# Kernel tuning notes

Measured on AMD Instinct MI355X. Metric: run time of the kernel, lower is better.

Reference implementation:

```python
import jax, jax.numpy as jnp
import numpy as np

A_DIM = 12      # action dim (half of augmented state)
N_STEPS = 10    # Heun ODE steps (Flow.N)
P = 0.95        # mixing coefficient in _Heun_method


def _mlp(x, obs, t, W1, b1, W2, b2, W3, b3, W4, b4):
    h = jnp.concatenate([x, obs, t], axis=-1)
    h = jnp.tanh(h @ W1 + b1)
    h = jnp.tanh(h @ W2 + b2)
    h = jnp.tanh(h @ W3 + b3)
    return h @ W4 + b4


def _heun(obs, x, params):
    # Flow._Heun_method: sequential Heun integration of the augmented state.
    z = x[..., :A_DIM]
    y = x[..., A_DIM:]
    dt = 1.0 / N_STEPS
    tshape = x.shape[:-1] + (1,)

    def step(carry, i):
        z, y = carry
        t = jnp.ones(tshape, x.dtype) * (i / N_STEPS)
        z_t = _mlp(y, obs, t, *params)
        z_in = z + z_t * dt
        y_t = _mlp(z_in, obs, t, *params)
        y_in = y + y_t * dt
        z_new = P * z_in + (1.0 - P) * y_in
        y_new = P * y_in + (1.0 - P) * z_new
        return (z_new, y_new), None

    (z, y), _ = jax.lax.scan(step, (z, y), jnp.arange(N_STEPS, dtype=x.dtype))
    return jnp.concatenate([z, y], axis=-1)


def setup_inputs() -> dict:
    key = jax.random.key(0)
    ks = jax.random.split(key, 8)
    B, OBS, H, A = 2048, 48, 256, A_DIM
    din = A + OBS + 1  # 61
    s = 0.05  # small init scale to keep tanh unsaturated
    return {
        "observations": jax.random.normal(ks[0], (B, OBS), jnp.float32),
        "action_aug_0": jax.random.normal(ks[1], (B, 2 * A), jnp.float32),
        "W1": s * jax.random.normal(ks[2], (din, H), jnp.float32),
        "b1": jnp.zeros((H,), jnp.float32),
        "W2": s * jax.random.normal(ks[3], (H, H), jnp.float32),
        "b2": jnp.zeros((H,), jnp.float32),
        "W3": s * jax.random.normal(ks[4], (H, H), jnp.float32),
        "b3": jnp.zeros((H,), jnp.float32),
        "W4": s * jax.random.normal(ks[5], (H, A), jnp.float32),
        "b4": jnp.zeros((A,), jnp.float32),
        "jac": 1,
    }


def reference(observations, action_aug_0, W1, b1, W2, b2, W3, b3, W4, b4, jac):
    params = (W1, b1, W2, b2, W3, b3, W4, b4)
    action_aug = _heun(observations, action_aug_0, params)
    d = action_aug_0.shape[-1]
    # Normal(0, I) log prob summed over dims
    log_probs = -0.5 * jnp.sum(action_aug_0 ** 2, axis=-1) - 0.5 * d * jnp.log(2.0 * jnp.pi)
    if jac:
        single = lambda o, x: _heun(o, x, params)  # per-sample (obs_dim,), (2a,)
        J = jax.vmap(jax.jacrev(single, argnums=1))(observations, action_aug_0)  # (B, 2a, 2a)
        _, logabsdet = jnp.linalg.slogdet(J)  # = log|det J|
        log_probs = log_probs - logabsdet
    return action_aug, log_probs
```

## Files before the change

### kernel.cpp

```cpp
#include <hip/hip_runtime.h>
#include <hip/hip_bf16.h>


typedef unsigned short ushort_t;
typedef float f32x4 __attribute__((ext_vector_type(4)));
typedef short s16x8 __attribute__((ext_vector_type(8)));

#define NB      2048
#define OBS_D   48
#define XDIM    24
#define NSTEPS  10
#define DT      0.1f
#define PP      0.95f
#define SCL     2.885390081777927f

#define W1U  0
#define W2U  16384
#define W3U  81920
#define W4U  147456
#define W1AU 151552
#define FRAG_BLOCKS 624
#define LP_BLOCKS 8

#define LDS_BUFA 0
#define LDS_BUFB 8192
#define LDS_AIN  16384
#define LDS_PART 17408
#define LDS_TOTAL 25600

__device__ __forceinline__ ushort_t f2bf(float f) {
  unsigned u = __builtin_bit_cast(unsigned, f);
  u += 0x7fffu + ((u >> 16) & 1u);
  return (ushort_t)(u >> 16);
}

__device__ __forceinline__ float tanh_s(float u) {
  float e = __builtin_amdgcn_exp2f(u);
  return __builtin_fmaf(-2.f, __builtin_amdgcn_rcpf(1.f + e), 1.f);
}

__device__ __forceinline__ int pair_byte(int c) {
  return (((c >> 5) << 6) | ((c & 15) << 2) | (((c >> 4) & 1) << 1));
}

__global__ void prep_kernel(const float* __restrict__ W1, const float* __restrict__ b1,
                            const float* __restrict__ W2, const float* __restrict__ W3,
                            const float* __restrict__ W4, const float* __restrict__ x0,
                            const int* __restrict__ jac, float* __restrict__ out,
                            ushort_t* __restrict__ ws) {
  int bid = blockIdx.x;
  int tid = threadIdx.x;
  if (bid < FRAG_BLOCKS) {
    int e = bid * 256 + tid;
    float val = 0.f;
    if (e < 16384) {
      int kt = e >> 13; int r = e & 8191;
      int nt = r >> 9, l = (r >> 3) & 63, j = r & 7;
      int k = kt * 32 + ((l >> 4) << 2) + (j >> 1) + ((j & 1) << 4);
      int col = nt * 16 + (l & 15);
      val = SCL * ((k < 61) ? W1[k * 256 + col] : ((k == 61) ? b1[col] : 0.f));
    } else if (e < 81920) {
      int e2 = e - 16384;
      int kt = e2 >> 13; int r = e2 & 8191;
      int nt = r >> 9, l = (r >> 3) & 63, j = r & 7;
      int k = kt * 32 + ((l >> 4) << 2) + (j >> 1) + ((j & 1) << 4);
      val = SCL * W2[k * 256 + nt * 16 + (l & 15)];
    } else if (e < 147456) {
      int e2 = e - 81920;
      int kt = e2 >> 13; int r = e2 & 8191;
      int nt = r >> 9, l = (r >> 3) & 63, j = r & 7;
      int k = kt * 32 + ((l >> 4) << 2) + (j >> 1) + ((j & 1) << 4);
      val = SCL * W3[k * 256 + nt * 16 + (l & 15)];
    } else if (e < 151552) {
      int e2 = e - 147456;
      int kt = e2 >> 9; int r = e2 & 511;
      int l = (r >> 3) & 63, j = r & 7;
      int k = kt * 32 + ((l >> 4) << 2) + (j >> 1) + ((j & 1) << 4);
      int col = l & 15;
      val = (col < 12) ? W4[k * 12 + col] : 0.f;
    } else {
      int e2 = e - 151552;
      int nt = e2 >> 9; int r = e2 & 511;
      int l = (r >> 3) & 63, j = r & 7;
      int k = ((l >> 4) << 2) + (j >> 1) + ((j & 1) << 4);
      val = (k < 12) ? SCL * W1[k * 256 + nt * 16 + (l & 15)] : 0.f;
    }
    ws[e] = f2bf(val);
  } else {
    int s = (bid - FRAG_BLOCKS) * 256 + tid;
    float acc = 0.f;
    #pragma unroll 4
    for (int j = 0; j < XDIM; ++j) { float v = x0[s * XDIM + j]; acc += v * v; }
    float C = (jac[0] != 0) ? -9.744134143900015f : -22.054524796912143f;
    out[NB * XDIM + s] = -0.5f * acc + C;
  }
}

__global__ __launch_bounds__(512, 2) void flow_main(
    const float* __restrict__ obs, const float* __restrict__ x0,
    const float* __restrict__ W1g, const float* __restrict__ b2g,
    const float* __restrict__ b3g, const float* __restrict__ b4g,
    const ushort_t* __restrict__ ws, float* __restrict__ out) {
  __shared__ char lds[LDS_TOTAL];
  const int tid  = threadIdx.x;
  const int lane = tid & 63;
  const int wv   = tid >> 6;
  const int g    = lane >> 4;
  const int ar   = lane & 15;
  const int row0 = blockIdx.x * 16;
  const int sw   = (ar & 7) << 4;
  const int rs   = tid >> 4, cs = tid & 15;

  int roff[8];
  #pragma unroll
  for (int c = 0; c < 8; ++c)
    roff[c] = ar * 512 + (((((wv + c) & 7) * 64) + g * 16) ^ sw);
  int woff[4], pwoff[4];
  #pragma unroll
  for (int r = 0; r < 4; ++r) {
    int rw = 4 * g + r;
    woff[r]  = rw * 512 + ((wv * 64 + ar * 4) ^ ((rw & 7) << 4));
    pwoff[r] = LDS_PART + ((rw * 128 + ar * 8 + (wv ^ (g << 1))) << 2);
  }

  ((unsigned*)(lds + LDS_BUFB))[tid] = 0u;
  if (tid < 256) ((unsigned*)(lds + LDS_AIN))[tid] = 0u;
  __syncthreads();

  for (int idx = tid; idx < 16 * OBS_D; idx += 512) {
    int r = idx / OBS_D, o = idx - r * OBS_D;
    int byt = pair_byte(12 + o) ^ ((r & 7) << 4);
    *(ushort_t*)(lds + LDS_BUFB + r * 128 + byt) = f2bf(obs[(row0 + r) * OBS_D + o]);
  }
  if (tid < 16)
    *(ushort_t*)(lds + LDS_BUFB + tid * 128 + (pair_byte(61) ^ ((tid & 7) << 4))) = (ushort_t)0x3F80;

  float zr = 0.f, yr = 0.f, zir = 0.f;
  if (tid < 256 && cs < 12) {
    zr = x0[(row0 + rs) * XDIM + cs];
    yr = x0[(row0 + rs) * XDIM + 12 + cs];
    *(ushort_t*)(lds + LDS_AIN + rs * 64 + ((cs * 4) ^ ((rs & 3) << 4))) = f2bf(yr);
  }

  s16x8 w1o[2][2], w1a[2], w2r[8][2], w3r[8][2], w4r;
  #pragma unroll
  for (int kt = 0; kt < 2; ++kt)
    #pragma unroll
    for (int n = 0; n < 2; ++n)
      w1o[kt][n] = *(const s16x8*)(ws + W1U + (((kt * 16) + (2 * wv + n)) * 64 + lane) * 8);
  #pragma unroll
  for (int n = 0; n < 2; ++n)
    w1a[n] = *(const s16x8*)(ws + W1AU + ((2 * wv + n) * 64 + lane) * 8);
  #pragma unroll
  for (int c = 0; c < 8; ++c) {
    int kt = (wv + c) & 7;
    #pragma unroll
    for (int n = 0; n < 2; ++n) {
      w2r[c][n] = *(const s16x8*)(ws + W2U + (((kt * 16) + (2 * wv + n)) * 64 + lane) * 8);
      w3r[c][n] = *(const s16x8*)(ws + W3U + (((kt * 16) + (2 * wv + n)) * 64 + lane) * 8);
    }
  }
  w4r = *(const s16x8*)(ws + W4U + (wv * 64 + lane) * 8);
  asm volatile("" : "+v"(w1a[0]), "+v"(w1a[1]), "+v"(w4r));
  #pragma unroll
  for (int c = 0; c < 8; ++c)
    asm volatile("" : "+v"(w2r[c][0]), "+v"(w2r[c][1]), "+v"(w3r[c][0]), "+v"(w3r[c][1]));

  const float w1t0 = SCL * W1g[60 * 256 + 32 * wv + ar];
  const float w1t1 = SCL * W1g[60 * 256 + 32 * wv + 16 + ar];
  const float b2s0 = SCL * b2g[32 * wv + ar],      b2s1 = SCL * b2g[32 * wv + 16 + ar];
  const float b3s0 = SCL * b3g[32 * wv + ar],      b3s1 = SCL * b3g[32 * wv + 16 + ar];
  const float b4v  = (cs < 12) ? b4g[cs] : 0.f;

  __syncthreads();

  const f32x4 z4 = {0.f, 0.f, 0.f, 0.f};
  f32x4 ci0 = z4, ci1 = z4;
  #pragma unroll
  for (int kt = 0; kt < 2; ++kt) {
    s16x8 a = *(const s16x8*)(lds + LDS_BUFB + ar * 128 + ((kt * 64 + g * 16) ^ sw));
    ci0 = __builtin_amdgcn_mfma_f32_16x16x32_bf16(a, w1o[kt][0], ci0, 0, 0, 0);
    ci1 = __builtin_amdgcn_mfma_f32_16x16x32_bf16(a, w1o[kt][1], ci1, 0, 0, 0);
  }

  for (int i = 0; i < NSTEPS; ++i) {
    const float t = (float)i * DT;
    const float t0 = t * w1t0, t1 = t * w1t1;
    #pragma unroll
    for (int ev = 0; ev < 2; ++ev) {
      f32x4 acc0 = ci0, acc1 = ci1;
      #pragma unroll
      for (int r = 0; r < 4; ++r) { acc0[r] += t0; acc1[r] += t1; }
      {
        s16x8 a = *(const s16x8*)(lds + LDS_AIN + ar * 64 + ((g * 16) ^ ((ar & 3) << 4)));
        acc0 = __builtin_amdgcn_mfma_f32_16x16x32_bf16(a, w1a[0], acc0, 0, 0, 0);
        acc1 = __builtin_amdgcn_mfma_f32_16x16x32_bf16(a, w1a[1], acc1, 0, 0, 0);
      }
      #pragma unroll
      for (int r = 0; r < 4; ++r) {
        unsigned p;
        float lo = tanh_s(acc0[r]), hi = tanh_s(acc1[r]);
        asm("v_cvt_pk_bf16_f32 %0, %1, %2" : "=v"(p) : "v"(lo), "v"(hi));
        *(unsigned*)(lds + LDS_BUFA + woff[r]) = p;
      }
      __syncthreads();

      f32x4 c0[4], c1[4];
      c0[0] = (f32x4){b2s0, b2s0, b2s0, b2s0}; c1[0] = (f32x4){b2s1, b2s1, b2s1, b2s1};
      c0[1] = z4; c0[2] = z4; c0[3] = z4; c1[1] = z4; c1[2] = z4; c1[3] = z4;
      __builtin_amdgcn_s_setprio(1);
      #pragma unroll
      for (int c = 0; c < 4; ++c) {
        s16x8 a = *(const s16x8*)(lds + LDS_BUFA + roff[c]);
        s16x8 b = *(const s16x8*)(lds + LDS_BUFA + roff[c + 4]);
        c0[c] = __builtin_amdgcn_mfma_f32_16x16x32_bf16(a, w2r[c][0], c0[c], 0, 0, 0);
        c1[c] = __builtin_amdgcn_mfma_f32_16x16x32_bf16(a, w2r[c][1], c1[c], 0, 0, 0);
        c0[c] = __builtin_amdgcn_mfma_f32_16x16x32_bf16(b, w2r[c + 4][0], c0[c], 0, 0, 0);
        c1[c] = __builtin_amdgcn_mfma_f32_16x16x32_bf16(b, w2r[c + 4][1], c1[c], 0, 0, 0);
      }
      __builtin_amdgcn_s_setprio(0);
      acc0 = (c0[0] + c0[1]) + (c0[2] + c0[3]);
      acc1 = (c1[0] + c1[1]) + (c1[2] + c1[3]);
      #pragma unroll
      for (int r = 0; r < 4; ++r) {
        unsigned p;
        float lo = tanh_s(acc0[r]), hi = tanh_s(acc1[r]);
        asm("v_cvt_pk_bf16_f32 %0, %1, %2" : "=v"(p) : "v"(lo), "v"(hi));
        *(unsigned*)(lds + LDS_BUFB + woff[r]) = p;
      }
      __syncthreads();

      c0[0] = (f32x4){b3s0, b3s0, b3s0, b3s0}; c1[0] = (f32x4){b3s1, b3s1, b3s1, b3s1};
      c0[1] = z4; c0[2] = z4; c0[3] = z4; c1[1] = z4; c1[2] = z4; c1[3] = z4;
      __builtin_amdgcn_s_setprio(1);
      #pragma unroll
      for (int c = 0; c < 4; ++c) {
        s16x8 a = *(const s16x8*)(lds + LDS_BUFB + roff[c]);
        s16x8 b = *(const s16x8*)(lds + LDS_BUFB + roff[c + 4]);
        c0[c] = __builtin_amdgcn_mfma_f32_16x16x32_bf16(a, w3r[c][0], c0[c], 0, 0, 0);
        c1[c] = __builtin_amdgcn_mfma_f32_16x16x32_bf16(a, w3r[c][1], c1[c], 0, 0, 0);
        c0[c] = __builtin_amdgcn_mfma_f32_16x16x32_bf16(b, w3r[c + 4][0], c0[c], 0, 0, 0);
        c1[c] = __builtin_amdgcn_mfma_f32_16x16x32_bf16(b, w3r[c + 4][1], c1[c], 0, 0, 0);
      }
      __builtin_amdgcn_s_setprio(0);
      acc0 = (c0[0] + c0[1]) + (c0[2] + c0[3]);
      acc1 = (c1[0] + c1[1]) + (c1[2] + c1[3]);
      #pragma unroll
      for (int r = 0; r < 4; ++r) {
        unsigned p;
        float lo = tanh_s(acc0[r]), hi = tanh_s(acc1[r]);
        asm("v_cvt_pk_bf16_f32 %0, %1, %2" : "=v"(p) : "v"(lo), "v"(hi));
        *(unsigned*)(lds + LDS_BUFA + woff[r]) = p;
      }

      asm volatile("s_waitcnt lgkmcnt(0)" ::: "memory");
      __builtin_amdgcn_sched_barrier(0);
      {
        s16x8 a = *(const s16x8*)(lds + LDS_BUFA + roff[0]);
        f32x4 p4 = __builtin_amdgcn_mfma_f32_16x16x32_bf16(a, w4r, z4, 0, 0, 0);
        #pragma unroll
        for (int r = 0; r < 4; ++r)
          *(float*)(lds + pwoff[r]) = p4[r];
      }
      __syncthreads();

      if (tid < 256) {
        const char* pb = lds + LDS_PART + ((rs * 128 + cs * 8) << 2);
        f32x4 va = *(const f32x4*)pb;
        f32x4 vb = *(const f32x4*)(pb + 16);
        f32x4 sv = va + vb;
        float s = ((sv[0] + sv[1]) + (sv[2] + sv[3])) + b4v;
        if (cs < 12) {
          int byt = rs * 64 + ((cs * 4) ^ ((rs & 3) << 4));
          if (ev == 0) {
            zir = zr + DT * s;
            *(ushort_t*)(lds + LDS_AIN + byt) = f2bf(zir);
          } else {
            float yi = yr + DT * s;
            zr = PP * zir + (1.f - PP) * yi;
            yr = PP * yi + (1.f - PP) * zr;
            *(ushort_t*)(lds + LDS_AIN + byt) = f2bf(yr);
          }
        }
      }
      __syncthreads();
    }
  }

  if (tid < 256 && cs < 12) {
    out[(row0 + rs) * XDIM + cs]      = zr;
    out[(row0 + rs) * XDIM + 12 + cs] = yr;
  }
}

extern "C" void kernel_launch(void* const* d_in, const int* in_sizes, int n_in,
                              void* d_out, int out_size, void* d_ws, size_t ws_size,
                              hipStream_t stream) {
  const float* obs = (const float*)d_in[0];
  const float* x0  = (const float*)d_in[1];
  const float* W1  = (const float*)d_in[2];
  const float* b1  = (const float*)d_in[3];
  const float* W2  = (const float*)d_in[4];
  const float* b2  = (const float*)d_in[5];
  const float* W3  = (const float*)d_in[6];
  const float* b3  = (const float*)d_in[7];
  const float* W4  = (const float*)d_in[8];
  const float* b4  = (const float*)d_in[9];
  const int*   jac = (const int*)d_in[10];
  float* out = (float*)d_out;
  ushort_t* ws = (ushort_t*)d_ws;

  prep_kernel<<<FRAG_BLOCKS + LP_BLOCKS, 256, 0, stream>>>(W1, b1, W2, W3, W4, x0, jac, out, ws);
  flow_main<<<128, 512, 0, stream>>>(obs, x0, W1, b2, b3, b4, ws, out);
}
```

Baseline: 47.20 us.

## Process two 16-row tiles per block to reuse register-resident weights

Each 512-thread block now handles 32 batch rows as two 16-row tiles instead of one, so the grid is halved. Per layer, the MFMAs and tanh work for both tiles are interleaved, which reuses the weight fragments already held in registers and gives independent MFMA chains to hide latency across each barrier. LDS buffers are doubled to hold both tiles, and every thread now takes part in the state update. The cost is half as many blocks on a large GPU, leaving fewer CUs busy, along with more registers and more LDS per block.

```diff
diff --git a/kernel.cpp b/kernel.cpp
--- a/kernel.cpp
+++ b/kernel.cpp
@@ -13,6 +13,7 @@
 #define DT      0.1f
 #define PP      0.95f
 #define SCL     2.885390081777927f
+#define TILES   2
 
 #define W1U  0
 #define W2U  16384
@@ -23,10 +24,10 @@
 #define LP_BLOCKS 8
 
 #define LDS_BUFA 0
-#define LDS_BUFB 8192
-#define LDS_AIN  16384
-#define LDS_PART 17408
-#define LDS_TOTAL 25600
+#define LDS_BUFB 16384
+#define LDS_AIN  32768
+#define LDS_PART 34816
+#define LDS_TOTAL 51200
 
 __device__ __forceinline__ ushort_t f2bf(float f) {
   unsigned u = __builtin_bit_cast(unsigned, f);
@@ -107,9 +108,9 @@
   const int wv   = tid >> 6;
   const int g    = lane >> 4;
   const int ar   = lane & 15;
-  const int row0 = blockIdx.x * 16;
+  const int row0 = blockIdx.x * (16 * TILES);
   const int sw   = (ar & 7) << 4;
-  const int rs   = tid >> 4, cs = tid & 15;
+  const int tt   = tid >> 8, rs = (tid >> 4) & 15, cs = tid & 15;
 
   int roff[8];
   #pragma unroll
@@ -123,23 +124,33 @@
     pwoff[r] = LDS_PART + ((rw * 128 + ar * 8 + (wv ^ (g << 1))) << 2);
   }
 
-  ((unsigned*)(lds + LDS_BUFB))[tid] = 0u;
-  if (tid < 256) ((unsigned*)(lds + LDS_AIN))[tid] = 0u;
+  {
+    unsigned* z1 = (unsigned*)(lds + LDS_BUFB);
+    unsigned* z2 = (unsigned*)(lds + LDS_BUFB + 8192);
+    if (tid < 512) { z1[tid] = 0u; z2[tid] = 0u; }
+    ((unsigned*)(lds + LDS_AIN))[tid] = 0u;
+  }
   __syncthreads();
 
-  for (int idx = tid; idx < 16 * OBS_D; idx += 512) {
-    int r = idx / OBS_D, o = idx - r * OBS_D;
+  for (int idx = tid; idx < TILES * 16 * OBS_D; idx += 512) {
+    int t = idx / (16 * OBS_D);
+    int rem = idx - t * (16 * OBS_D);
+    int r = rem / OBS_D, o = rem - r * OBS_D;
     int byt = pair_byte(12 + o) ^ ((r & 7) << 4);
-    *(ushort_t*)(lds + LDS_BUFB + r * 128 + byt) = f2bf(obs[(row0 + r) * OBS_D + o]);
-  }
-  if (tid < 16)
-    *(ushort_t*)(lds + LDS_BUFB + tid * 128 + (pair_byte(61) ^ ((tid & 7) << 4))) = (ushort_t)0x3F80;
+    *(ushort_t*)(lds + LDS_BUFB + t * 8192 + r * 128 + byt) =
+        f2bf(obs[(row0 + t * 16 + r) * OBS_D + o]);
+  }
+  if (tid < 16 * TILES) {
+    int t = tid >> 4, r = tid & 15;
+    *(ushort_t*)(lds + LDS_BUFB + t * 8192 + r * 128 + (pair_byte(61) ^ ((r & 7) << 4))) =
+        (ushort_t)0x3F80;
+  }
 
   float zr = 0.f, yr = 0.f, zir = 0.f;
-  if (tid < 256 && cs < 12) {
-    zr = x0[(row0 + rs) * XDIM + cs];
-    yr = x0[(row0 + rs) * XDIM + 12 + cs];
-    *(ushort_t*)(lds + LDS_AIN + rs * 64 + ((cs * 4) ^ ((rs & 3) << 4))) = f2bf(yr);
+  if (cs < 12) {
+    zr = x0[(row0 + tt * 16 + rs) * XDIM + cs];
+    yr = x0[(row0 + tt * 16 + rs) * XDIM + 12 + cs];
+    *(ushort_t*)(lds + LDS_AIN + tt * 1024 + rs * 64 + ((cs * 4) ^ ((rs & 3) << 4))) = f2bf(yr);
   }
 
   s16x8 w1o[2][2], w1a[2], w2r[8][2], w3r[8][2], w4r;
@@ -175,12 +186,16 @@
   __syncthreads();
 
   const f32x4 z4 = {0.f, 0.f, 0.f, 0.f};
-  f32x4 ci0 = z4, ci1 = z4;
-  #pragma unroll
-  for (int kt = 0; kt < 2; ++kt) {
-    s16x8 a = *(const s16x8*)(lds + LDS_BUFB + ar * 128 + ((kt * 64 + g * 16) ^ sw));
-    ci0 = __builtin_amdgcn_mfma_f32_16x16x32_bf16(a, w1o[kt][0], ci0, 0, 0, 0);
-    ci1 = __builtin_amdgcn_mfma_f32_16x16x32_bf16(a, w1o[kt][1], ci1, 0, 0, 0);
+  f32x4 ci0[TILES], ci1[TILES];
+  #pragma unroll
+  for (int t = 0; t < TILES; ++t) {
+    ci0[t] = z4; ci1[t] = z4;
+    #pragma unroll
+    for (int kt = 0; kt < 2; ++kt) {
+      s16x8 a = *(const s16x8*)(lds + LDS_BUFB + t * 8192 + ar * 128 + ((kt * 64 + g * 16) ^ sw));
+      ci0[t] = __builtin_amdgcn_mfma_f32_16x16x32_bf16(a, w1o[kt][0], ci0[t], 0, 0, 0);
+      ci1[t] = __builtin_amdgcn_mfma_f32_16x16x32_bf16(a, w1o[kt][1], ci1[t], 0, 0, 0);
+    }
   }
 
   for (int i = 0; i < NSTEPS; ++i) {
@@ -188,90 +203,112 @@
     const float t0 = t * w1t0, t1 = t * w1t1;
     #pragma unroll
     for (int ev = 0; ev < 2; ++ev) {
-      f32x4 acc0 = ci0, acc1 = ci1;
-      #pragma unroll
-      for (int r = 0; r < 4; ++r) { acc0[r] += t0; acc1[r] += t1; }
-      {
-        s16x8 a = *(const s16x8*)(lds + LDS_AIN + ar * 64 + ((g * 16) ^ ((ar & 3) << 4)));
-        acc0 = __builtin_amdgcn_mfma_f32_16x16x32_bf16(a, w1a[0], acc0, 0, 0, 0);
-        acc1 = __builtin_amdgcn_mfma_f32_16x16x32_bf16(a, w1a[1], acc1, 0, 0, 0);
-      }
-      #pragma unroll
-      for (int r = 0; r < 4; ++r) {
-        unsigned p;
-        float lo = tanh_s(acc0[r]), hi = tanh_s(acc1[r]);
-        asm("v_cvt_pk_bf16_f32 %0, %1, %2" : "=v"(p) : "v"(lo), "v"(hi));
-        *(unsigned*)(lds + LDS_BUFA + woff[r]) = p;
-      }
+      f32x4 acc0[TILES], acc1[TILES];
+      #pragma unroll
+      for (int tl = 0; tl < TILES; ++tl) {
+        acc0[tl] = ci0[tl]; acc1[tl] = ci1[tl];
+        #pragma unroll
+        for (int r = 0; r < 4; ++r) { acc0[tl][r] += t0; acc1[tl][r] += t1; }
+        s16x8 a = *(const s16x8*)(lds + LDS_AIN + tl * 1024 + ar * 64 +
+                                  ((g * 16) ^ ((ar & 3) << 4)));
+        acc0[tl] = __builtin_amdgcn_mfma_f32_16x16x32_bf16(a, w1a[0], acc0[tl], 0, 0, 0);
+        acc1[tl] = __builtin_amdgcn_mfma_f32_16x16x32_bf16(a, w1a[1], acc1[tl], 0, 0, 0);
+      }
+      #pragma unroll
+      for (int tl = 0; tl < TILES; ++tl)
+        #pragma unroll
+        for (int r = 0; r < 4; ++r) {
+          unsigned p;
+          float lo = tanh_s(acc0[tl][r]), hi = tanh_s(acc1[tl][r]);
+          asm("v_cvt_pk_bf16_f32 %0, %1, %2" : "=v"(p) : "v"(lo), "v"(hi));
+          *(unsigned*)(lds + LDS_BUFA + tl * 8192 + woff[r]) = p;
+        }
       __syncthreads();
 
-      f32x4 c0[4], c1[4];
-      c0[0] = (f32x4){b2s0, b2s0, b2s0, b2s0}; c1[0] = (f32x4){b2s1, b2s1, b2s1, b2s1};
-      c0[1] = z4; c0[2] = z4; c0[3] = z4; c1[1] = z4; c1[2] = z4; c1[3] = z4;
+      f32x4 A0a[TILES], A0b[TILES], A1a[TILES], A1b[TILES];
+      #pragma unroll
+      for (int tl = 0; tl < TILES; ++tl) {
+        A0a[tl] = (f32x4){b2s0, b2s0, b2s0, b2s0};
+        A1a[tl] = (f32x4){b2s1, b2s1, b2s1, b2s1};
+        A0b[tl] = z4; A1b[tl] = z4;
+      }
       __builtin_amdgcn_s_setprio(1);
       #pragma unroll
-      for (int c = 0; c < 4; ++c) {
-        s16x8 a = *(const s16x8*)(lds + LDS_BUFA + roff[c]);
-        s16x8 b = *(const s16x8*)(lds + LDS_BUFA + roff[c + 4]);
-        c0[c] = __builtin_amdgcn_mfma_f32_16x16x32_bf16(a, w2r[c][0], c0[c], 0, 0, 0);
-        c1[c] = __builtin_amdgcn_mfma_f32_16x16x32_bf16(a, w2r[c][1], c1[c], 0, 0, 0);
-        c0[c] = __builtin_amdgcn_mfma_f32_16x16x32_bf16(b, w2r[c + 4][0], c0[c], 0, 0, 0);
-        c1[c] = __builtin_amdgcn_mfma_f32_16x16x32_bf16(b, w2r[c + 4][1], c1[c], 0, 0, 0);
-      }
+      for (int c = 0; c < 4; ++c)
+        #pragma unroll
+        for (int tl = 0; tl < TILES; ++tl) {
+          s16x8 a = *(const s16x8*)(lds + LDS_BUFA + tl * 8192 + roff[c]);
+          s16x8 b = *(const s16x8*)(lds + LDS_BUFA + tl * 8192 + roff[c + 4]);
+          A0a[tl] = __builtin_amdgcn_mfma_f32_16x16x32_bf16(a, w2r[c][0], A0a[tl], 0, 0, 0);
+          A1a[tl] = __builtin_amdgcn_mfma_f32_16x16x32_bf16(a, w2r[c][1], A1a[tl], 0, 0, 0);
+          A0b[tl] = __builtin_amdgcn_mfma_f32_16x16x32_bf16(b, w2r[c + 4][0], A0b[tl], 0, 0, 0);
+          A1b[tl] = __builtin_amdgcn_mfma_f32_16x16x32_bf16(b, w2r[c + 4][1], A1b[tl], 0, 0, 0);
+        }
       __builtin_amdgcn_s_setprio(0);
-      acc0 = (c0[0] + c0[1]) + (c0[2] + c0[3]);
-      acc1 = (c1[0] + c1[1]) + (c1[2] + c1[3]);
-      #pragma unroll
-      for (int r = 0; r < 4; ++r) {
-        unsigned p;
-        float lo = tanh_s(acc0[r]), hi = tanh_s(acc1[r]);
-        asm("v_cvt_pk_bf16_f32 %0, %1, %2" : "=v"(p) : "v"(lo), "v"(hi));
-        *(unsigned*)(lds + LDS_BUFB + woff[r]) = p;
+      #pragma unroll
+      for (int tl = 0; tl < TILES; ++tl) {
+        acc0[tl] = A0a[tl] + A0b[tl]; acc1[tl] = A1a[tl] + A1b[tl];
+        #pragma unroll
+        for (int r = 0; r < 4; ++r) {
+          unsigned p;
+          float lo = tanh_s(acc0[tl][r]), hi = tanh_s(acc1[tl][r]);
+          asm("v_cvt_pk_bf16_f32 %0, %1, %2" : "=v"(p) : "v"(lo), "v"(hi));
+          *(unsigned*)(lds + LDS_BUFB + tl * 8192 + woff[r]) = p;
+        }
       }
       __syncthreads();
 
-      c0[0] = (f32x4){b3s0, b3s0, b3s0, b3s0}; c1[0] = (f32x4){b3s1, b3s1, b3s1, b3s1};
-      c0[1] = z4; c0[2] = z4; c0[3] = z4; c1[1] = z4; c1[2] = z4; c1[3] = z4;
+      #pragma unroll
+      for (int tl = 0; tl < TILES; ++tl) {
+        A0a[tl] = (f32x4){b3s0, b3s0, b3s0, b3s0};
+        A1a[tl] = (f32x4){b3s1, b3s1, b3s1, b3s1};
+        A0b[tl] = z4; A1b[tl] = z4;
+      }
       __builtin_amdgcn_s_setprio(1);
       #pragma unroll
-      for (int c = 0; c < 4; ++c) {
-        s16x8 a = *(const s16x8*)(lds + LDS_BUFB + roff[c]);
-        s16x8 b = *(const s16x8*)(lds + LDS_BUFB + roff[c + 4]);
-        c0[c] = __builtin_amdgcn_mfma_f32_16x16x32_bf16(a, w3r[c][0], c0[c], 0, 0, 0);
-        c1[c] = __builtin_amdgcn_mfma_f32_16x16x32_bf16(a, w3r[c][1], c1[c], 0, 0, 0);
-        c0[c] = __builtin_amdgcn_mfma_f32_16x16x32_bf16(b, w3r[c + 4][0], c0[c], 0, 0, 0);
-        c1[c] = __builtin_amdgcn_mfma_f32_16x16x32_bf16(b, w3r[c + 4][1], c1[c], 0, 0, 0);
-      }
+      for (int c = 0; c < 4; ++c)
+        #pragma unroll
+        for (int tl = 0; tl < TILES; ++tl) {
+          s16x8 a = *(const s16x8*)(lds + LDS_BUFB + tl * 8192 + roff[c]);
+          s16x8 b = *(const s16x8*)(lds + LDS_BUFB + tl * 8192 + roff[c + 4]);
+          A0a[tl] = __builtin_amdgcn_mfma_f32_16x16x32_bf16(a, w3r[c][0], A0a[tl], 0, 0, 0);
+          A1a[tl] = __builtin_amdgcn_mfma_f32_16x16x32_bf16(a, w3r[c][1], A1a[tl], 0, 0, 0);
+          A0b[tl] = __builtin_amdgcn_mfma_f32_16x16x32_bf16(b, w3r[c + 4][0], A0b[tl], 0, 0, 0);
+          A1b[tl] = __builtin_amdgcn_mfma_f32_16x16x32_bf16(b, w3r[c + 4][1], A1b[tl], 0, 0, 0);
+        }
       __builtin_amdgcn_s_setprio(0);
-      acc0 = (c0[0] + c0[1]) + (c0[2] + c0[3]);
-      acc1 = (c1[0] + c1[1]) + (c1[2] + c1[3]);
-      #pragma unroll
-      for (int r = 0; r < 4; ++r) {
-        unsigned p;
-        float lo = tanh_s(acc0[r]), hi = tanh_s(acc1[r]);
-        asm("v_cvt_pk_bf16_f32 %0, %1, %2" : "=v"(p) : "v"(lo), "v"(hi));
-        *(unsigned*)(lds + LDS_BUFA + woff[r]) = p;
+      #pragma unroll
+      for (int tl = 0; tl < TILES; ++tl) {
+        acc0[tl] = A0a[tl] + A0b[tl]; acc1[tl] = A1a[tl] + A1b[tl];
+        #pragma unroll
+        for (int r = 0; r < 4; ++r) {
+          unsigned p;
+          float lo = tanh_s(acc0[tl][r]), hi = tanh_s(acc1[tl][r]);
+          asm("v_cvt_pk_bf16_f32 %0, %1, %2" : "=v"(p) : "v"(lo), "v"(hi));
+          *(unsigned*)(lds + LDS_BUFA + tl * 8192 + woff[r]) = p;
+        }
       }
 
       asm volatile("s_waitcnt lgkmcnt(0)" ::: "memory");
       __builtin_amdgcn_sched_barrier(0);
+      #pragma unroll
+      for (int tl = 0; tl < TILES; ++tl) {
+        s16x8 a = *(const s16x8*)(lds + LDS_BUFA + tl * 8192 + roff[0]);
+        f32x4 p4 = __builtin_amdgcn_mfma_f32_16x16x32_bf16(a, w4r, z4, 0, 0, 0);
+        #pragma unroll
+        for (int r = 0; r < 4; ++r)
+          *(float*)(lds + tl * 8192 + pwoff[r]) = p4[r];
+      }
+      __syncthreads();
+
       {
-        s16x8 a = *(const s16x8*)(lds + LDS_BUFA + roff[0]);
-        f32x4 p4 = __builtin_amdgcn_mfma_f32_16x16x32_bf16(a, w4r, z4, 0, 0, 0);
-        #pragma unroll
-        for (int r = 0; r < 4; ++r)
-          *(float*)(lds + pwoff[r]) = p4[r];
-      }
-      __syncthreads();
-
-      if (tid < 256) {
-        const char* pb = lds + LDS_PART + ((rs * 128 + cs * 8) << 2);
+        const char* pb = lds + LDS_PART + tt * 8192 + ((rs * 128 + cs * 8) << 2);
         f32x4 va = *(const f32x4*)pb;
         f32x4 vb = *(const f32x4*)(pb + 16);
         f32x4 sv = va + vb;
         float s = ((sv[0] + sv[1]) + (sv[2] + sv[3])) + b4v;
         if (cs < 12) {
-          int byt = rs * 64 + ((cs * 4) ^ ((rs & 3) << 4));
+          int byt = tt * 1024 + rs * 64 + ((cs * 4) ^ ((rs & 3) << 4));
           if (ev == 0) {
             zir = zr + DT * s;
             *(ushort_t*)(lds + LDS_AIN + byt) = f2bf(zir);
@@ -287,9 +324,9 @@
     }
   }
 
-  if (tid < 256 && cs < 12) {
-    out[(row0 + rs) * XDIM + cs]      = zr;
-    out[(row0 + rs) * XDIM + 12 + cs] = yr;
+  if (cs < 12) {
+    out[(row0 + tt * 16 + rs) * XDIM + cs]      = zr;
+    out[(row0 + tt * 16 + rs) * XDIM + 12 + cs] = yr;
   }
 }
 
@@ -311,5 +348,5 @@
   ushort_t* ws = (ushort_t*)d_ws;
 
   prep_kernel<<<FRAG_BLOCKS + LP_BLOCKS, 256, 0, stream>>>(W1, b1, W2, W3, W4, x0, jac, out, ws);
-  flow_main<<<128, 512, 0, stream>>>(obs, x0, W1, b2, b3, b4, ws, out);
-}
+  flow_main<<<NB / (16 * TILES), 512, 0, stream>>>(obs, x0, W1, b2, b3, b4, ws, out);
+}
```

Result: slower. 73.46 us (+55.6%).
